# Kernel tuning notes

Hardware: AMD Instinct MI355X
Metric: run time of the kernel (lower is better)

The kernel has to match this reference:

```python
import jax, jax.numpy as jnp
import numpy as np

B, N, E = 2, 25000, 400000
FC_IN, FC_HID = 64, 256
MUL = 32                     # multiplicity of each output irrep (0e,1e,2e)
W_NUMEL = 3 * MUL            # 96 tensor-product weights per edge
NUM_NEIGHBORS = 16.0


def setup_inputs() -> dict:
    key = jax.random.key(0)
    k1, k2, k3, k4, k5, k6 = jax.random.split(key, 6)
    return {
        "edge_src": jax.random.randint(k1, (E,), 0, N),
        "edge_dst": jax.random.randint(k2, (E,), 0, N),
        "node_emb": jax.random.normal(k3, (B, N, 3), jnp.float32),
        "edge_type": jax.random.normal(k4, (E, FC_IN), jnp.float32),
        "W1": jax.random.normal(k5, (FC_IN, FC_HID), jnp.float32),
        "W2": jax.random.normal(k6, (FC_HID, W_NUMEL), jnp.float32),
    }


def _tensor_product(x, y, w):
    """1o x 1o -> 32x0e + 32x1e + 32x2e, per-edge uvw weights.
    x, y: (B,E,3); w: (E,96). Component-normalized CG coefficients."""
    inv3 = 1.0 / np.sqrt(3.0)
    inv2 = 1.0 / np.sqrt(2.0)
    inv6 = 1.0 / np.sqrt(6.0)
    w0, w1, w2 = w[:, :MUL], w[:, MUL:2 * MUL], w[:, 2 * MUL:]
    # l=0 path: dot product
    s = jnp.sum(x * y, axis=-1) * inv3                     # (B,E)
    out0 = w0[None] * s[..., None]                         # (B,E,32)
    # l=1 path: cross product
    v = jnp.cross(x, y) * inv2                             # (B,E,3)
    out1 = (w1[None, :, :, None] * v[:, :, None, :]).reshape(B, E, 3 * MUL)
    # l=2 path: symmetric traceless combinations
    x0, x1, x2 = x[..., 0], x[..., 1], x[..., 2]
    y0, y1, y2 = y[..., 0], y[..., 1], y[..., 2]
    t = jnp.stack([
        (x0 * y1 + x1 * y0) * inv2,
        (x1 * y2 + x2 * y1) * inv2,
        (x0 * y2 + x2 * y0) * inv2,
        (x0 * y0 - x1 * y1) * inv2,
        (2.0 * x2 * y2 - x0 * y0 - x1 * y1) * inv6,
    ], axis=-1)                                            # (B,E,5)
    out2 = (w2[None, :, :, None] * t[:, :, None, :]).reshape(B, E, 5 * MUL)
    return jnp.concatenate([out0, out1, out2], axis=-1)    # (B,E,288)


def reference(edge_src, edge_dst, node_emb, edge_type, W1, W2):
    # per-edge FC generating TP weights (e3nn FullyConnectedNet-style fan-in norm)
    h = jax.nn.silu(edge_type @ W1 * (1.0 / np.sqrt(FC_IN)))   # (E,256)
    w = (h @ W2) * (1.0 / np.sqrt(FC_HID))                     # (E,96)
    src_emb = node_emb[:, edge_src]                            # (B,E,3)
    dst_emb = node_emb[:, edge_dst]                            # (B,E,3)
    edge_message = _tensor_product(src_emb, dst_emb, w)        # (B,E,288)
    out = jnp.zeros((B, N, edge_message.shape[-1]), edge_message.dtype)
    out = out.at[:, edge_dst].add(edge_message)                # scatter-sum over dst
    return out * (1.0 / np.sqrt(NUM_NEIGHBORS))
```

## Files before the change

### kernel.cpp

```cpp
#include <hip/hip_runtime.h>

#define EDGES 400000
#define NN 25000
#define NCH 288
#define EPA 64
#define NBIN_PAD 25024
#define SWS 68

#define W1FRAG 16384
#define W2FRAG 24576

typedef float f32x4 __attribute__((ext_vector_type(4)));
typedef short short8 __attribute__((ext_vector_type(8)));

__device__ __forceinline__ unsigned short f2bf(float x) {
    unsigned u = __float_as_uint(x);
    unsigned r = (u + 0x7fffu + ((u >> 16) & 1u)) >> 16;
    return (unsigned short)r;
}
__device__ __forceinline__ unsigned short f2bf_t(float x) {
    return (unsigned short)(__float_as_uint(x) >> 16);
}
__device__ __forceinline__ float bf2f(unsigned short h) {
    return __uint_as_float(((unsigned)h) << 16);
}
__device__ __forceinline__ unsigned cvtpk(float a, float b) {
    unsigned r;
    asm("v_cvt_pk_bf16_f32 %0, %1, %2" : "=v"(r) : "v"(a), "v"(b));
    return r;
}
__device__ __forceinline__ float lowf(unsigned u)  { return __uint_as_float(u << 16); }
__device__ __forceinline__ float highf(unsigned u) { return __uint_as_float(u & 0xffff0000u); }

__global__ void k_wfrag(const float* __restrict__ W1, const float* __restrict__ W2,
                        unsigned short* __restrict__ w1h, unsigned short* __restrict__ w1l,
                        unsigned short* __restrict__ w2h, unsigned short* __restrict__ w2l) {
    int i = blockIdx.x * 256 + threadIdx.x;
    if (i < W1FRAG) {
        int j = i & 7, l = (i >> 3) & 63, nt = (i >> 9) & 15, k2 = (i >> 13) & 1;
        int n = nt * 16 + (l & 15), k = k2 * 32 + ((l >> 4) * 8) + j;
        float v = W1[k * 256 + n] * 0.125f;
        unsigned short hb = f2bf(v);
        w1h[i] = hb; w1l[i] = f2bf_t(v - bf2f(hb));
    } else if (i < W1FRAG + W2FRAG) {
        int i2 = i - W1FRAG;
        int j = i2 & 7, l = (i2 >> 3) & 63, r = i2 >> 9;
        int nt = r % 6, k8 = r / 6;
        int n = nt * 16 + (l & 15), k = k8 * 32 + ((l >> 4) * 8) + j;
        float v = W2[k * 96 + n] * 0.015625f;
        unsigned short hb = f2bf(v);
        w2h[i2] = hb; w2l[i2] = f2bf_t(v - bf2f(hb));
    }
}

__global__ void k_hist(const int* __restrict__ edst, unsigned* __restrict__ cnt) {
    int i = blockIdx.x * 256 + threadIdx.x;
    if (i < EDGES) atomicAdd(&cnt[edst[i]], 1u);
}

__global__ __launch_bounds__(1024) void k_scanA(const unsigned* __restrict__ cnt,
                                                unsigned* __restrict__ cur,
                                                unsigned* __restrict__ tot) {
    __shared__ unsigned s_wt[16];
    const int t = threadIdx.x, lane = t & 63, wid = t >> 6;
    int i = blockIdx.x * 1024 + t;
    unsigned v = (i < NN) ? cnt[i] : 0u;
    unsigned incl = v;
    #pragma unroll
    for (int d = 1; d < 64; d <<= 1) {
        unsigned u = __shfl_up(incl, d);
        if (lane >= d) incl += u;
    }
    if (lane == 63) s_wt[wid] = incl;
    __syncthreads();
    if (wid == 0 && lane < 16) {
        unsigned wincl = s_wt[lane];
        #pragma unroll
        for (int d = 1; d < 16; d <<= 1) {
            unsigned u = __shfl_up(wincl, d);
            if (lane >= d) wincl += u;
        }
        s_wt[lane] = wincl;
    }
    __syncthreads();
    unsigned waveoff = (wid > 0) ? s_wt[wid - 1] : 0u;
    if (i < NN) cur[i] = waveoff + incl - v;
    if (t == 0) tot[blockIdx.x] = s_wt[15];
}

__global__ void k_scanB(unsigned* __restrict__ tot, unsigned* __restrict__ toff, int nblk) {
    int lane = threadIdx.x;
    unsigned v = (lane < nblk) ? tot[lane] : 0u;
    unsigned incl = v;
    #pragma unroll
    for (int d = 1; d < 64; d <<= 1) {
        unsigned u = __shfl_up(incl, d);
        if (lane >= d) incl += u;
    }
    if (lane < nblk) toff[lane] = incl - v;
}

__global__ __launch_bounds__(1024) void k_scanC(unsigned* __restrict__ cur,
                                                const unsigned* __restrict__ toff) {
    int i = blockIdx.x * 1024 + threadIdx.x;
    if (i < NN) cur[i] += toff[blockIdx.x];
}

__global__ void k_perm(const int* __restrict__ edst, unsigned* __restrict__ cur,
                       unsigned* __restrict__ perm) {
    int i = blockIdx.x * 256 + threadIdx.x;
    if (i < EDGES) {
        unsigned p = atomicAdd(&cur[edst[i]], 1u);
        perm[p] = (unsigned)i;
    }
}

struct SMemU {
    union {
        struct __align__(16) {
            unsigned short a1h[EPA * 64];
            unsigned short a1l[EPA * 64];
            unsigned short a2h[EPA * 64];
            unsigned short a2l[EPA * 64];
        };
        float sw[96 * SWS];
    };
};

template <bool SORTED>
__global__ __launch_bounds__(256) void conv_fused(
    const int* __restrict__ esrc, const int* __restrict__ edst,
    const float* __restrict__ nemb, const float* __restrict__ etype,
    const unsigned short* __restrict__ w1h, const unsigned short* __restrict__ w1l,
    const unsigned short* __restrict__ w2h, const unsigned short* __restrict__ w2l,
    const unsigned* __restrict__ perm,
    float* __restrict__ out)
{
    __shared__ SMemU U;
    __shared__ __align__(16) float gsm[2][9][SWS];
    __shared__ int s_eidx[EPA], s_dst[EPA];
    __shared__ unsigned s_mlo, s_mhi;

    const int t = threadIdx.x;
    const int lane = t & 63, w = t >> 6;
    const int g = lane >> 4, ln15 = lane & 15;
    const size_t slot0 = (size_t)blockIdx.x * EPA;

    if (t < EPA) {
        int e = SORTED ? (int)perm[slot0 + t] : (int)(slot0 + t);
        s_eidx[t] = e;
        s_dst[t] = edst[e];
    }
    __syncthreads();

    #pragma unroll
    for (int i = 0; i < 4; ++i) {
        int f4 = t + 256 * i;
        int row = f4 >> 4, q = f4 & 15;
        const float4* src = (const float4*)(etype + (size_t)s_eidx[row] * 64);
        float4 v = src[q];
        unsigned hp01 = cvtpk(v.x, v.y), hp23 = cvtpk(v.z, v.w);
        float lo0 = v.x - lowf(hp01), lo1 = v.y - highf(hp01);
        float lo2 = v.z - lowf(hp23), lo3 = v.w - highf(hp23);
        unsigned lp01 = cvtpk(lo0, lo1), lp23 = cvtpk(lo2, lo3);
        int boff = row * 128 + ((q * 8) ^ ((row & 7) << 4));
        *(uint2*)((char*)U.a1h + boff) = make_uint2(hp01, hp23);
        *(uint2*)((char*)U.a1l + boff) = make_uint2(lp01, lp23);
    }
    if (t < EPA * 2) {
        int e = t >> 1, b = t & 1;
        int sn = esrc[s_eidx[e]], dn = s_dst[e];
        const float* xp = nemb + ((size_t)b * NN + sn) * 3;
        const float* yp = nemb + ((size_t)b * NN + dn) * 3;
        float x0 = xp[0], x1 = xp[1], x2 = xp[2];
        float y0 = yp[0], y1 = yp[1], y2 = yp[2];
        const float inv3 = 0.5773502691896258f;
        const float inv2 = 0.7071067811865476f;
        const float inv6 = 0.4082482904638630f;
        gsm[b][0][e] = (x0*y0 + x1*y1 + x2*y2) * inv3;
        gsm[b][1][e] = (x1*y2 - x2*y1) * inv2;
        gsm[b][2][e] = (x2*y0 - x0*y2) * inv2;
        gsm[b][3][e] = (x0*y1 - x1*y0) * inv2;
        gsm[b][4][e] = (x0*y1 + x1*y0) * inv2;
        gsm[b][5][e] = (x1*y2 + x2*y1) * inv2;
        gsm[b][6][e] = (x0*y2 + x2*y0) * inv2;
        gsm[b][7][e] = (x0*y0 - x1*y1) * inv2;
        gsm[b][8][e] = (2.0f*x2*y2 - x0*y0 - x1*y1) * inv6;
    } else if (t < 192) {
        int e = t - 128;
        bool flag = (e > 0) && (s_dst[e] != s_dst[e - 1]);
        unsigned long long bal = __ballot(flag);
        if (e == 0) { s_mlo = (unsigned)bal; s_mhi = (unsigned)(bal >> 32); }
    }
    __syncthreads();

    const int mh = w & 1, nb = 3 * (w >> 1);
    f32x4 acc2[2][3];
    #pragma unroll
    for (int mm = 0; mm < 2; ++mm)
        #pragma unroll
        for (int n = 0; n < 3; ++n)
            #pragma unroll
            for (int r = 0; r < 4; ++r) acc2[mm][n][r] = 0.f;

    #pragma unroll
    for (int qt = 0; qt < 4; ++qt) {
        f32x4 acc1[4];
        #pragma unroll
        for (int m = 0; m < 4; ++m)
            #pragma unroll
            for (int r = 0; r < 4; ++r) acc1[m][r] = 0.f;

        #pragma unroll
        for (int k2 = 0; k2 < 2; ++k2) {
            int idx = ((k2 * 16 + 4 * qt + w) * 64 + lane) * 8;
            short8 wah = *(const short8*)(w1h + idx);
            short8 wal = *(const short8*)(w1l + idx);
            #pragma unroll
            for (int m = 0; m < 4; ++m) {
                int row = m * 16 + ln15;
                int boff = row * 128 + (((k2 * 64) + g * 16) ^ ((row & 7) << 4));
                short8 eth = *(const short8*)((const char*)U.a1h + boff);
                short8 etl = *(const short8*)((const char*)U.a1l + boff);
                acc1[m] = __builtin_amdgcn_mfma_f32_16x16x32_bf16(wah, eth, acc1[m], 0, 0, 0);
                acc1[m] = __builtin_amdgcn_mfma_f32_16x16x32_bf16(wal, eth, acc1[m], 0, 0, 0);
                acc1[m] = __builtin_amdgcn_mfma_f32_16x16x32_bf16(wah, etl, acc1[m], 0, 0, 0);
            }
        }

        #pragma unroll
        for (int m = 0; m < 4; ++m) {
            float p0 = acc1[m][0], p1 = acc1[m][1], p2 = acc1[m][2], p3 = acc1[m][3];
            float s0 = p0 * __builtin_amdgcn_rcpf(1.f + __expf(-p0));
            float s1 = p1 * __builtin_amdgcn_rcpf(1.f + __expf(-p1));
            float s2 = p2 * __builtin_amdgcn_rcpf(1.f + __expf(-p2));
            float s3 = p3 * __builtin_amdgcn_rcpf(1.f + __expf(-p3));
            unsigned hp0 = cvtpk(s0, s1), hp1 = cvtpk(s2, s3);
            float lo0 = s0 - lowf(hp0), lo1 = s1 - highf(hp0);
            float lo2 = s2 - lowf(hp1), lo3 = s3 - highf(hp1);
            unsigned lp0 = cvtpk(lo0, lo1), lp1 = cvtpk(lo2, lo3);
            int e = m * 16 + ln15;
            int boff = e * 128 + ((w * 32 + g * 8) ^ ((ln15 & 7) << 4));
            *(uint2*)((char*)U.a2h + boff) = make_uint2(hp0, hp1);
            *(uint2*)((char*)U.a2l + boff) = make_uint2(lp0, lp1);
        }
        __syncthreads();

        #pragma unroll
        for (int kk = 0; kk < 2; ++kk) {
            int kg = 2 * qt + kk;
            short8 bh[3], bl[3];
            #pragma unroll
            for (int n = 0; n < 3; ++n) {
                int idx = ((kg * 6 + nb + n) * 64 + lane) * 8;
                bh[n] = *(const short8*)(w2h + idx);
                bl[n] = *(const short8*)(w2l + idx);
            }
            #pragma unroll
            for (int mm = 0; mm < 2; ++mm) {
                int row = (2 * mh + mm) * 16 + ln15;
                int boff = row * 128 + ((kk * 64 + g * 16) ^ ((ln15 & 7) << 4));
                short8 ah = *(const short8*)((const char*)U.a2h + boff);
                short8 al = *(const short8*)((const char*)U.a2l + boff);
                #pragma unroll
                for (int n = 0; n < 3; ++n) {
                    acc2[mm][n] = __builtin_amdgcn_mfma_f32_16x16x32_bf16(ah, bh[n], acc2[mm][n], 0, 0, 0);
                    acc2[mm][n] = __builtin_amdgcn_mfma_f32_16x16x32_bf16(ah, bl[n], acc2[mm][n], 0, 0, 0);
                    acc2[mm][n] = __builtin_amdgcn_mfma_f32_16x16x32_bf16(al, bh[n], acc2[mm][n], 0, 0, 0);
                }
            }
        }
        __syncthreads();
    }

    #pragma unroll
    for (int mm = 0; mm < 2; ++mm) {
        #pragma unroll
        for (int n = 0; n < 3; ++n) {
            int c = (nb + n) * 16 + ln15;
            int e_base = (2 * mh + mm) * 16 + g * 4;
            *(f32x4*)&U.sw[c * SWS + e_base] = acc2[mm][n];
        }
    }
    __syncthreads();

    {
        unsigned mlo = __builtin_amdgcn_readfirstlane(s_mlo);
        unsigned mhi = __builtin_amdgcn_readfirstlane(s_mhi);
        for (int idx = t; idx < NCH * 2; idx += 256) {
            int b = idx >= NCH;
            int c = idx - b * NCH;
            unsigned wi, gi;
            if (c < 32)       { wi = c;                          gi = 0; }
            else if (c < 128) { unsigned q = c - 32;  wi = 32 + q / 3u; gi = 1 + q % 3u; }
            else              { unsigned q = c - 128; wi = 64 + q / 5u; gi = 4 + q % 5u; }
            float* base = out + (size_t)b * NN * NCH + c;
            float acc = 0.f;
            int rs = 0;
            #pragma unroll
            for (int q4 = 0; q4 < 16; ++q4) {
                f32x4 wv = *(const f32x4*)&U.sw[wi * SWS + q4 * 4];
                f32x4 gv = *(const f32x4*)&gsm[b][gi][q4 * 4];
                unsigned word = (q4 < 8) ? mlo : mhi;
                unsigned nib = (word >> ((q4 * 4) & 31)) & 0xFu;
                if (nib == 0u) {
                    acc = fmaf(wv[0], gv[0], acc);
                    acc = fmaf(wv[1], gv[1], acc);
                    acc = fmaf(wv[2], gv[2], acc);
                    acc = fmaf(wv[3], gv[3], acc);
                } else {
                    #pragma unroll
                    for (int j = 0; j < 4; ++j) {
                        int e = q4 * 4 + j;
                        if (e && ((nib >> j) & 1u)) {
                            float* addr = base + (size_t)s_dst[e - 1] * NCH;
                            if (SORTED && rs > 0) *addr = acc;
                            else atomicAdd(addr, acc);
                            acc = 0.f; rs = e;
                        }
                        acc = fmaf(wv[j], gv[j], acc);
                    }
                }
            }
            atomicAdd(base + (size_t)s_dst[EPA - 1] * NCH, acc);
        }
    }
}

extern "C" void kernel_launch(void* const* d_in, const int* in_sizes, int n_in,
                              void* d_out, int out_size, void* d_ws, size_t ws_size,
                              hipStream_t stream) {
    const int*   esrc  = (const int*)d_in[0];
    const int*   edst  = (const int*)d_in[1];
    const float* nemb  = (const float*)d_in[2];
    const float* etype = (const float*)d_in[3];
    const float* W1    = (const float*)d_in[4];
    const float* W2    = (const float*)d_in[5];
    float* out = (float*)d_out;

    hipMemsetAsync(out, 0, (size_t)out_size * sizeof(float), stream);

    const size_t frag_bytes = (size_t)(2 * W1FRAG + 2 * W2FRAG) * sizeof(unsigned short);
    unsigned short* w1h = (unsigned short*)d_ws;
    unsigned short* w1l = w1h + W1FRAG;
    unsigned short* w2h = w1l + W1FRAG;
    unsigned short* w2l = w2h + W2FRAG;

    const int NSCAN = (NN + 1023) / 1024;
    size_t o_cnt  = frag_bytes;
    size_t o_cur  = o_cnt + (size_t)NBIN_PAD * 4;
    size_t o_tot  = o_cur + (size_t)NBIN_PAD * 4;
    size_t o_toff = o_tot + 128;
    size_t o_perm = o_toff + 128;
    size_t need_sort = o_perm + (size_t)EDGES * 4;

    k_wfrag<<<(W1FRAG + W2FRAG + 255) / 256, 256, 0, stream>>>(W1, W2, w1h, w1l, w2h, w2l);

    if (ws_size >= need_sort) {
        unsigned* cnt  = (unsigned*)((char*)d_ws + o_cnt);
        unsigned* cur  = (unsigned*)((char*)d_ws + o_cur);
        unsigned* tot  = (unsigned*)((char*)d_ws + o_tot);
        unsigned* toff = (unsigned*)((char*)d_ws + o_toff);
        unsigned* perm = (unsigned*)((char*)d_ws + o_perm);
        hipMemsetAsync(cnt, 0, (size_t)NBIN_PAD * 4, stream);
        k_hist<<<(EDGES + 255) / 256, 256, 0, stream>>>(edst, cnt);
        k_scanA<<<NSCAN, 1024, 0, stream>>>(cnt, cur, tot);
        k_scanB<<<1, 64, 0, stream>>>(tot, toff, NSCAN);
        k_scanC<<<NSCAN, 1024, 0, stream>>>(cur, toff);
        k_perm<<<(EDGES + 255) / 256, 256, 0, stream>>>(edst, cur, perm);
        conv_fused<true><<<EDGES / EPA, 256, 0, stream>>>(
            esrc, edst, nemb, etype, w1h, w1l, w2h, w2l, perm, out);
    } else {
        conv_fused<false><<<EDGES / EPA, 256, 0, stream>>>(
            esrc, edst, nemb, etype, w1h, w1l, w2h, w2l, nullptr, out);
    }
}
```

Before: 197.4 us.

## Split hidden-layer phases into 8 narrower chunks to halve acc1 and a2 staging

The fused FC loop now runs over 8 phases of 32 hidden units instead of 4 phases of 64. Each wave computes 2 edge tiles for one 16-unit slice rather than 4 edge tiles. This halves the acc1 register footprint and the a2h/a2l shared staging buffers, and the LDS swizzle is changed to match the narrower layout. The goal is lower register and LDS pressure for better occupancy, at the cost of twice as many __syncthreads barriers per block.

```diff
diff --git a/kernel.cpp b/kernel.cpp
--- a/kernel.cpp
+++ b/kernel.cpp
@@ -120,8 +120,8 @@
         struct __align__(16) {
             unsigned short a1h[EPA * 64];
             unsigned short a1l[EPA * 64];
-            unsigned short a2h[EPA * 64];
-            unsigned short a2l[EPA * 64];
+            unsigned short a2h[EPA * 32];
+            unsigned short a2l[EPA * 32];
         };
         float sw[96 * SWS];
     };
@@ -195,6 +195,7 @@
     __syncthreads();
 
     const int mh = w & 1, nb = 3 * (w >> 1);
+    const int np = w & 1, ehf = w >> 1;
     f32x4 acc2[2][3];
     #pragma unroll
     for (int mm = 0; mm < 2; ++mm)
@@ -204,33 +205,33 @@
             for (int r = 0; r < 4; ++r) acc2[mm][n][r] = 0.f;
 
     #pragma unroll
-    for (int qt = 0; qt < 4; ++qt) {
-        f32x4 acc1[4];
-        #pragma unroll
-        for (int m = 0; m < 4; ++m)
-            #pragma unroll
-            for (int r = 0; r < 4; ++r) acc1[m][r] = 0.f;
+    for (int ph = 0; ph < 8; ++ph) {
+        f32x4 acc1[2];
+        #pragma unroll
+        for (int mi = 0; mi < 2; ++mi)
+            #pragma unroll
+            for (int r = 0; r < 4; ++r) acc1[mi][r] = 0.f;
 
         #pragma unroll
         for (int k2 = 0; k2 < 2; ++k2) {
-            int idx = ((k2 * 16 + 4 * qt + w) * 64 + lane) * 8;
+            int idx = ((k2 * 16 + 2 * ph + np) * 64 + lane) * 8;
             short8 wah = *(const short8*)(w1h + idx);
             short8 wal = *(const short8*)(w1l + idx);
             #pragma unroll
-            for (int m = 0; m < 4; ++m) {
-                int row = m * 16 + ln15;
+            for (int mi = 0; mi < 2; ++mi) {
+                int row = (2 * ehf + mi) * 16 + ln15;
                 int boff = row * 128 + (((k2 * 64) + g * 16) ^ ((row & 7) << 4));
                 short8 eth = *(const short8*)((const char*)U.a1h + boff);
                 short8 etl = *(const short8*)((const char*)U.a1l + boff);
-                acc1[m] = __builtin_amdgcn_mfma_f32_16x16x32_bf16(wah, eth, acc1[m], 0, 0, 0);
-                acc1[m] = __builtin_amdgcn_mfma_f32_16x16x32_bf16(wal, eth, acc1[m], 0, 0, 0);
-                acc1[m] = __builtin_amdgcn_mfma_f32_16x16x32_bf16(wah, etl, acc1[m], 0, 0, 0);
+                acc1[mi] = __builtin_amdgcn_mfma_f32_16x16x32_bf16(wah, eth, acc1[mi], 0, 0, 0);
+                acc1[mi] = __builtin_amdgcn_mfma_f32_16x16x32_bf16(wal, eth, acc1[mi], 0, 0, 0);
+                acc1[mi] = __builtin_amdgcn_mfma_f32_16x16x32_bf16(wah, etl, acc1[mi], 0, 0, 0);
             }
         }
 
         #pragma unroll
-        for (int m = 0; m < 4; ++m) {
-            float p0 = acc1[m][0], p1 = acc1[m][1], p2 = acc1[m][2], p3 = acc1[m][3];
+        for (int mi = 0; mi < 2; ++mi) {
+            float p0 = acc1[mi][0], p1 = acc1[mi][1], p2 = acc1[mi][2], p3 = acc1[mi][3];
             float s0 = p0 * __builtin_amdgcn_rcpf(1.f + __expf(-p0));
             float s1 = p1 * __builtin_amdgcn_rcpf(1.f + __expf(-p1));
             float s2 = p2 * __builtin_amdgcn_rcpf(1.f + __expf(-p2));
@@ -239,27 +240,25 @@
             float lo0 = s0 - lowf(hp0), lo1 = s1 - highf(hp0);
             float lo2 = s2 - lowf(hp1), lo3 = s3 - highf(hp1);
             unsigned lp0 = cvtpk(lo0, lo1), lp1 = cvtpk(lo2, lo3);
-            int e = m * 16 + ln15;
-            int boff = e * 128 + ((w * 32 + g * 8) ^ ((ln15 & 7) << 4));
+            int e = (2 * ehf + mi) * 16 + ln15;
+            int boff = e * 64 + ((np * 32 + g * 8) ^ ((e & 3) << 4));
             *(uint2*)((char*)U.a2h + boff) = make_uint2(hp0, hp1);
             *(uint2*)((char*)U.a2l + boff) = make_uint2(lp0, lp1);
         }
         __syncthreads();
 
-        #pragma unroll
-        for (int kk = 0; kk < 2; ++kk) {
-            int kg = 2 * qt + kk;
+        {
             short8 bh[3], bl[3];
             #pragma unroll
             for (int n = 0; n < 3; ++n) {
-                int idx = ((kg * 6 + nb + n) * 64 + lane) * 8;
+                int idx = ((ph * 6 + nb + n) * 64 + lane) * 8;
                 bh[n] = *(const short8*)(w2h + idx);
                 bl[n] = *(const short8*)(w2l + idx);
             }
             #pragma unroll
             for (int mm = 0; mm < 2; ++mm) {
                 int row = (2 * mh + mm) * 16 + ln15;
-                int boff = row * 128 + ((kk * 64 + g * 16) ^ ((ln15 & 7) << 4));
+                int boff = row * 64 + ((g * 16) ^ ((row & 3) << 4));
                 short8 ah = *(const short8*)((const char*)U.a2h + boff);
                 short8 al = *(const short8*)((const char*)U.a2l + boff);
                 #pragma unroll
```

After: 201.1 us. Within noise of the previous version (+1.9%).
